# Kernel optimization log

Measured on AMD Instinct MI355X. Metric: run time of the kernel, lower is better.

## Reference

```python
import jax, jax.numpy as jnp
import numpy as np

NUM_HEADS = 4
NUM_GROUPS = 8
EPS = 1e-5


def setup_inputs() -> dict:
    key = jax.random.key(0)
    ks = jax.random.split(key, 4)
    B, C, H, W = 4, 256, 64, 64
    x = jax.random.normal(ks[0], (B, C, H, W), dtype=jnp.float32)
    gamma = jnp.ones((C,), dtype=jnp.float32)
    beta = jnp.zeros((C,), dtype=jnp.float32)
    w_qkv = jax.random.normal(ks[1], (3 * C, C), dtype=jnp.float32) * 0.02
    b_qkv = jnp.zeros((3 * C,), dtype=jnp.float32)
    w_proj = jax.random.normal(ks[2], (C, C), dtype=jnp.float32) * 0.02
    b_proj = jnp.zeros((C,), dtype=jnp.float32)
    return {"x": x, "gamma": gamma, "beta": beta, "w_qkv": w_qkv,
            "b_qkv": b_qkv, "w_proj": w_proj, "b_proj": b_proj}


def _group_norm(x, gamma, beta):
    B, C, H, W = x.shape
    xg = x.reshape(B, NUM_GROUPS, C // NUM_GROUPS, H, W)
    mean = xg.mean(axis=(2, 3, 4), keepdims=True)
    var = xg.var(axis=(2, 3, 4), keepdims=True)
    xn = ((xg - mean) * jax.lax.rsqrt(var + EPS)).reshape(B, C, H, W)
    return xn * gamma[None, :, None, None] + beta[None, :, None, None]


def reference(x, gamma, beta, w_qkv, b_qkv, w_proj, b_proj):
    B, C, H, W = x.shape
    d = C // NUM_HEADS
    scale = d ** (-0.5)
    xn = _group_norm(x, gamma, beta)
    # 1x1 conv == per-pixel linear: (B,C,H,W) x (3C,C) -> (B,3C,H,W)
    qkv = jnp.einsum('bchw,oc->bohw', xn, w_qkv) + b_qkv[None, :, None, None]
    q, k, v = jnp.split(qkv, 3, axis=1)
    S = H * W
    q = q.reshape(B, NUM_HEADS, d, S)  # (B,h,d,S)
    k = k.reshape(B, NUM_HEADS, d, S)
    v = v.reshape(B, NUM_HEADS, d, S)
    # attn scores: q^T k, scaled AFTER the matmul (as in source)
    attn = jax.nn.softmax(jnp.einsum('bhds,bhdt->bhst', q, k) * scale, axis=-1)
    # out = attn @ v^T -> (B,h,S,d) then transpose to (B,h,d,S) -> (B,C,H,W)
    out = jnp.einsum('bhst,bhdt->bhds', attn, v).reshape(B, C, H, W)
    y = jnp.einsum('bchw,oc->bohw', out, w_proj) + b_proj[None, :, None, None]
    return x + y
```

## Files before the change

### kernel.cpp

```cpp
#include <hip/hip_runtime.h>
#include <hip/hip_bf16.h>


typedef __attribute__((ext_vector_type(8))) short          b16x8;
typedef __attribute__((ext_vector_type(4))) float          f32x4;
typedef __attribute__((ext_vector_type(4))) unsigned short u16x4;
typedef __attribute__((ext_vector_type(8))) unsigned short u16x8;

#define SWZ(row, chunk) (((chunk) ^ ((row) & 7)))

__device__ __forceinline__ unsigned short f2bf(float f) {
    union { float f; unsigned u; } v; v.f = f;
    unsigned r = v.u + 0x7FFF + ((v.u >> 16) & 1);
    return (unsigned short)(r >> 16);
}

__device__ __forceinline__ float bf2f(unsigned short u) {
    union { unsigned u; float f; } v; v.u = ((unsigned)u) << 16;
    return v.f;
}

__device__ __forceinline__ unsigned bfpack_trunc(float lo, float hi) {
    union { float f; unsigned u; } a, b;
    a.f = hi; b.f = lo;
    return __builtin_amdgcn_perm(a.u, b.u, 0x07060302u);
}

__device__ __forceinline__ float fexp2(float x) {
#if __has_builtin(__builtin_amdgcn_exp2f)
    return __builtin_amdgcn_exp2f(x);
#else
    return exp2f(x);
#endif
}

__device__ __forceinline__ float frcp(float x) {
#if __has_builtin(__builtin_amdgcn_rcpf)
    return __builtin_amdgcn_rcpf(x);
#else
    return 1.f / x;
#endif
}

__device__ __forceinline__ void gll16(const void* g, void* l) {
    __builtin_amdgcn_global_load_lds(
        (const __attribute__((address_space(1))) unsigned int*)g,
        (__attribute__((address_space(3))) unsigned int*)l, 16, 0, 0);
}

__global__ __launch_bounds__(256) void gn_prepack(const float* __restrict__ x,
                                                  float* __restrict__ partials,
                                                  const float* __restrict__ wqkv,
                                                  const float* __restrict__ bqkv,
                                                  unsigned short* __restrict__ wsw,
                                                  float* __restrict__ bq_pre,
                                                  const float* __restrict__ wproj,
                                                  unsigned short* __restrict__ wswp) {
    int bx = blockIdx.x;
    int t = threadIdx.x;
    if (bx < 512) {
        int bg = bx >> 4, part = bx & 15;
        const float* xp = x + (size_t)bg * 131072 + (size_t)part * 8192;
        float s = 0.f, ss = 0.f;
        for (int k = 0; k < 8; k++) {
            float4 v = *(const float4*)(xp + t * 4 + k * 1024);
            s += v.x + v.y + v.z + v.w;
            ss += v.x * v.x + v.y * v.y + v.z * v.z + v.w * v.w;
        }
        for (int off = 32; off; off >>= 1) {
            s += __shfl_down(s, off);
            ss += __shfl_down(ss, off);
        }
        __shared__ float rs[4], rss[4];
        if ((t & 63) == 0) { rs[t >> 6] = s; rss[t >> 6] = ss; }
        __syncthreads();
        if (t == 0) {
            partials[2 * bx]     = rs[0] + rs[1] + rs[2] + rs[3];
            partials[2 * bx + 1] = rss[0] + rss[1] + rss[2] + rss[3];
        }
    } else if (bx < 608) {
        int gid = (bx - 512) * 256 + t;
        const float qs = 0.125f * 1.44269504f;
        int o = gid >> 5, ch = gid & 31, cblk = ch >> 3, chl = ch & 7;
        float sc = (o < 256) ? qs : 1.f;
        const float* src = &wqkv[o * 256 + ch * 8];
        u16x8 v;
        for (int i = 0; i < 8; i++) v[i] = f2bf(src[i] * sc);
        *(u16x8*)&wsw[((cblk * 768 + o) << 6) + SWZ(o, chl) * 8] = v;
        if (gid < 768) bq_pre[gid] = bqkv[gid] * ((gid < 256) ? qs : 1.f);
    } else {
        int gid = (bx - 608) * 256 + t;
        int o = gid >> 5, ch = gid & 31, cblk = ch >> 3, chl = ch & 7;
        const float* src = &wproj[o * 256 + ch * 8];
        u16x8 v;
        for (int i = 0; i < 8; i++) v[i] = f2bf(src[i]);
        *(u16x8*)&wswp[((cblk * 256 + o) << 6) + SWZ(o, chl) * 8] = v;
    }
}

__global__ __launch_bounds__(256) void qkv_gemm(const float* __restrict__ x,
                                                const float* __restrict__ gamma,
                                                const float* __restrict__ beta,
                                                const unsigned short* __restrict__ wsw,
                                                const float* __restrict__ bq_pre,
                                                const float* __restrict__ partials,
                                                unsigned short* __restrict__ qT,
                                                unsigned short* __restrict__ kT,
                                                unsigned short* __restrict__ vT) {
    __shared__ __align__(16) unsigned short Asm[256 * 64];
    __shared__ __align__(16) unsigned short Bsm[64 * 72];
    __shared__ float stats_s[16];
    int s0 = blockIdx.x * 64, sec = blockIdx.y, b = blockIdx.z;
    int t = threadIdx.x, lane = t & 63, wv = t >> 6;
    int l15 = lane & 15, quad = lane >> 4;
    f32x4 acc[4][4] = {};

    if (t < 8) {
        float s = 0.f, ss = 0.f;
        for (int p = 0; p < 16; p++) {
            s  += partials[2 * ((b * 8 + t) * 16 + p)];
            ss += partials[2 * ((b * 8 + t) * 16 + p) + 1];
        }
        const float invN = 1.f / 131072.f;
        float mean = s * invN;
        float var = ss * invN - mean * mean;
        stats_s[2 * t] = mean;
        stats_s[2 * t + 1] = rsqrtf(var + 1e-5f);
    }

    int tc = t >> 5;
    int ts = (t & 31) * 2;

    for (int k0 = 0; k0 < 256; k0 += 64) {
        int cblk = k0 >> 6;
        __syncthreads();
        const unsigned short* asrc = wsw + (((size_t)cblk * 768 + sec * 256) << 6);
        for (int j = 0; j < 8; j++) {
            int blk = wv * 8 + j;
            gll16(asrc + blk * 512 + lane * 8, &Asm[blk * 512]);
        }
        {
            int cbase = k0 + tc * 8;
            int g = cbase >> 5;
            float mean = stats_s[2 * g], rstd = stats_s[2 * g + 1];
            u16x8 r0, r1;
            for (int ci = 0; ci < 8; ci++) {
                int c = cbase + ci;
                float2 xv = *(const float2*)&x[((size_t)(b * 256 + c)) * 4096 + s0 + ts];
                float ga = gamma[c] * rstd, be = beta[c] - mean * gamma[c] * rstd;
                r0[ci] = (short)f2bf(xv.x * ga + be);
                r1[ci] = (short)f2bf(xv.y * ga + be);
            }
            *(u16x8*)&Bsm[(ts + 0) * 72 + tc * 8] = r0;
            *(u16x8*)&Bsm[(ts + 1) * 72 + tc * 8] = r1;
        }
        __syncthreads();
        for (int kc = 0; kc < 2; kc++) {
            b16x8 bb[4];
            for (int nn = 0; nn < 4; nn++)
                bb[nn] = *(const b16x8*)(Bsm + (nn * 16 + l15) * 72 + kc * 32 + quad * 8);
            for (int ot = 0; ot < 4; ot++) {
                int row = wv * 16 + l15;
                b16x8 a = *(const b16x8*)&Asm[(ot * 64 + row) * 64 + SWZ(row, kc * 4 + quad) * 8];
                for (int nn = 0; nn < 4; nn++)
                    acc[ot][nn] = __builtin_amdgcn_mfma_f32_16x16x32_bf16(a, bb[nn], acc[ot][nn], 0, 0, 0);
            }
        }
    }

    if (sec < 2) {
        unsigned short* dstT = (sec == 0) ? qT : kT;
        int ddbase = wv * 16 + quad * 4;
        for (int ot = 0; ot < 4; ot++) {
            unsigned short* dst = dstT + (size_t)(b * 4 + ot) * 4096 * 64;
            for (int nn = 0; nn < 4; nn++) {
                int s = s0 + nn * 16 + l15;
                u16x4 pv;
                for (int r = 0; r < 4; r++)
                    pv[r] = f2bf(acc[ot][nn][r] + bq_pre[sec * 256 + ot * 64 + ddbase + r]);
                *(u16x4*)&dst[(size_t)s * 64 + SWZ(s, ddbase >> 3) * 8 + (ddbase & 7)] = pv;
            }
        }
    } else {
        int kt = blockIdx.x;
        for (int ot = 0; ot < 4; ot++) {
            int bh = b * 4 + ot;
            for (int r = 0; r < 4; r++) {
                int dd = wv * 16 + quad * 4 + r;
                float bs = bq_pre[512 + ot * 64 + dd];
                u16x4 pv = { f2bf(acc[ot][0][r] + bs), f2bf(acc[ot][1][r] + bs),
                             f2bf(acc[ot][2][r] + bs), f2bf(acc[ot][3][r] + bs) };
                size_t off = ((size_t)(bh * 64 + kt) * 64 + dd) * 64
                           + SWZ(dd, l15 >> 1) * 8 + (l15 & 1) * 4;
                *(u16x4*)&vT[off] = pv;
            }
        }
    }
}

__global__ __launch_bounds__(128, 2) void attn_kernel(const unsigned short* __restrict__ qT,
                                                      const unsigned short* __restrict__ kT,
                                                      const unsigned short* __restrict__ vT,
                                                      unsigned short* __restrict__ Opart,
                                                      float* __restrict__ lsum) {
    __shared__ __align__(16) unsigned short QP[128 * 64];
    __shared__ __align__(16) unsigned short Ksm[2][64 * 64];
    int bx = blockIdx.x;
    int q0 = (bx >> 1) * 128;
    int half = bx & 1;
    int kt0 = half * 32, ktN = kt0 + 32;
    int h = blockIdx.y, b = blockIdx.z;
    int bh = b * 4 + h, slab = bh * 2 + half;
    int t = threadIdx.x, lane = t & 63, wv = t >> 6;
    int l15 = lane & 15, quad = lane >> 4;

    const unsigned short* qTb = qT + (size_t)bh * 4096 * 64;
    const unsigned short* kTb = kT + (size_t)bh * 4096 * 64;
    const unsigned short* vTb = vT + (size_t)bh * 64 * 4096;

    for (int j = 0; j < 12; j++) {
        int i = wv + 2 * j;
        if (i < 16) {
            gll16(qTb + (size_t)q0 * 64 + i * 512 + lane * 8, &QP[i * 512]);
        } else {
            int ii = i - 16;
            gll16(kTb + (size_t)kt0 * 4096 + ii * 512 + lane * 8, &Ksm[0][ii * 512]);
        }
    }
    __syncthreads();

    b16x8 aq[4][2];
    for (int mt = 0; mt < 4; mt++)
        for (int kc = 0; kc < 2; kc++) {
            int row = wv * 64 + mt * 16 + l15;
            aq[mt][kc] = *(const b16x8*)&QP[row * 64 + SWZ(row, kc * 4 + quad) * 8];
        }

    f32x4 O[4][4] = {};
    float ls[4][4] = {};

    for (int kt = kt0; kt < ktN; kt++) {
        int cur = kt & 1;
        int nb = cur ^ 1;
        bool more = (kt < ktN - 1);
        if (more) {
            for (int j = 0; j < 4; j++) {
                int blk = wv * 4 + j;
                gll16(kTb + (size_t)(kt + 1) * 4096 + blk * 512 + lane * 8,
                      &Ksm[nb][blk * 512]);
            }
        }

        f32x4 sc[4][4] = {};
        for (int kc = 0; kc < 2; kc++) {
            b16x8 bk[4];
            for (int nk = 0; nk < 4; nk++) {
                int row = nk * 16 + l15;
                bk[nk] = *(const b16x8*)&Ksm[cur][row * 64 + SWZ(l15, kc * 4 + quad) * 8];
            }
            for (int mt = 0; mt < 4; mt++)
                for (int nk = 0; nk < 4; nk++)
                    sc[mt][nk] = __builtin_amdgcn_mfma_f32_16x16x32_bf16(
                        aq[mt][kc], bk[nk], sc[mt][nk], 0, 0, 0);
        }

        for (int mt = 0; mt < 4; mt++) {
            for (int r = 0; r < 4; r++) {
                float p0 = fexp2(sc[mt][0][r]);
                float p1 = fexp2(sc[mt][1][r]);
                float p2 = fexp2(sc[mt][2][r]);
                float p3 = fexp2(sc[mt][3][r]);
                ls[mt][r] += (p0 + p1) + (p2 + p3);
                int row = wv * 64 + mt * 16 + quad * 4 + r;
                u16x4 pk;
                pk[0] = (unsigned short)(bfpack_trunc(p0, p1) & 0xFFFF);
                union { unsigned u[2]; u16x4 v; } pku;
                pku.u[0] = bfpack_trunc(p0, p1);
                pku.u[1] = bfpack_trunc(p2, p3);
                *(u16x4*)&QP[row * 64 + SWZ(row, l15 >> 1) * 8 + (l15 & 1) * 4] = pku.v;
            }
        }

        for (int kc = 0; kc < 2; kc++) {
            b16x8 ap[4], bv[4];
            for (int mt = 0; mt < 4; mt++) {
                int row = wv * 64 + mt * 16 + l15;
                ap[mt] = *(const b16x8*)&QP[row * 64 + SWZ(row, kc * 4 + quad) * 8];
            }
            for (int nf = 0; nf < 4; nf++) {
                int row = nf * 16 + l15;
                bv[nf] = *(const b16x8*)&vTb[(size_t)kt * 4096 + row * 64
                                             + SWZ(l15, kc * 4 + quad) * 8];
            }
            for (int mt = 0; mt < 4; mt++)
                for (int nf = 0; nf < 4; nf++)
                    O[mt][nf] = __builtin_amdgcn_mfma_f32_16x16x32_bf16(
                        ap[mt], bv[nf], O[mt][nf], 0, 0, 0);
        }

        __syncthreads();
    }

    for (int mt = 0; mt < 4; mt++)
        for (int r = 0; r < 4; r++) {
            float s = ls[mt][r];
            for (int off = 1; off < 16; off <<= 1) s += __shfl_xor(s, off);
            int srow = q0 + wv * 64 + mt * 16 + quad * 4 + r;
            if (l15 == 0) lsum[(size_t)slab * 4096 + srow] = s;
        }

    for (int mt = 0; mt < 4; mt++)
        for (int nf = 0; nf < 4; nf++)
            for (int r = 0; r < 4; r++) {
                int s = q0 + wv * 64 + mt * 16 + quad * 4 + r;
                int d = nf * 16 + l15;
                Opart[((size_t)slab * 4096 + s) * 64 + d] = f2bf(O[mt][nf][r]);
            }
}

__global__ __launch_bounds__(256) void proj_gemm(const unsigned short* __restrict__ Opart,
                                                 const float* __restrict__ lsum,
                                                 const unsigned short* __restrict__ wswp,
                                                 const float* __restrict__ bias,
                                                 const float* __restrict__ x,
                                                 float* __restrict__ out) {
    __shared__ __align__(16) unsigned short Asm[64 * 64];
    __shared__ __align__(16) unsigned short Bsm[64 * 72];
    int s0 = blockIdx.x * 64, o0 = blockIdx.y * 64, b = blockIdx.z;
    int t = threadIdx.x, lane = t & 63, wv = t >> 6;
    int l15 = lane & 15, quad = lane >> 4;
    int rl = t >> 2;
    f32x4 acc[4] = {};
    for (int k0 = 0; k0 < 256; k0 += 64) {
        int cblk = k0 >> 6;
        __syncthreads();
        const unsigned short* asrc = wswp + (((size_t)cblk * 256 + o0) << 6);
        for (int j = 0; j < 2; j++) {
            int blk = wv * 2 + j;
            gll16(asrc + blk * 512 + lane * 8, &Asm[blk * 512]);
        }
        {
            int bh = b * 4 + cblk;
            int s = s0 + rl;
            float l0 = lsum[(size_t)(bh * 2 + 0) * 4096 + s];
            float l1 = lsum[(size_t)(bh * 2 + 1) * 4096 + s];
            float rcp = frcp(l0 + l1);
            for (int j = 0; j < 2; j++) {
                int off = (t & 3) * 16 + j * 8;
                u16x8 o0v = *(const u16x8*)&Opart[((size_t)(bh * 2 + 0) * 4096 + s) * 64 + off];
                u16x8 o1v = *(const u16x8*)&Opart[((size_t)(bh * 2 + 1) * 4096 + s) * 64 + off];
                u16x8 res;
                for (int i = 0; i < 8; i++)
                    res[i] = f2bf((bf2f(o0v[i]) + bf2f(o1v[i])) * rcp);
                *(u16x8*)&Bsm[rl * 72 + off] = res;
            }
        }
        __syncthreads();
        for (int kc = 0; kc < 2; kc++) {
            int row = wv * 16 + l15;
            b16x8 a = *(const b16x8*)&Asm[row * 64 + SWZ(row, kc * 4 + quad) * 8];
            for (int nn = 0; nn < 4; nn++) {
                b16x8 bb = *(const b16x8*)(Bsm + (nn * 16 + l15) * 72 + kc * 32 + quad * 8);
                acc[nn] = __builtin_amdgcn_mfma_f32_16x16x32_bf16(a, bb, acc[nn], 0, 0, 0);
            }
        }
    }
    for (int nn = 0; nn < 4; nn++) {
        for (int r = 0; r < 4; r++) {
            int o = o0 + wv * 16 + quad * 4 + r;
            int s = s0 + nn * 16 + l15;
            size_t idx = ((size_t)(b * 256 + o)) * 4096 + s;
            out[idx] = acc[nn][r] + bias[o] + x[idx];
        }
    }
}

extern "C" void kernel_launch(void* const* d_in, const int* in_sizes, int n_in,
                              void* d_out, int out_size, void* d_ws, size_t ws_size,
                              hipStream_t stream) {
    const float* x      = (const float*)d_in[0];
    const float* gamma  = (const float*)d_in[1];
    const float* beta   = (const float*)d_in[2];
    const float* w_qkv  = (const float*)d_in[3];
    const float* b_qkv  = (const float*)d_in[4];
    const float* w_proj = (const float*)d_in[5];
    const float* b_proj = (const float*)d_in[6];
    float* out = (float*)d_out;

    unsigned short* ws = (unsigned short*)d_ws;
    unsigned short* qT    = ws;
    unsigned short* kT    = qT + (size_t)16 * 4096 * 64;
    unsigned short* vT    = kT + (size_t)16 * 4096 * 64;
    unsigned short* scratch = vT + (size_t)16 * 4096 * 64;
    unsigned short* Opart = scratch + (size_t)4 * 4096 * 256;
    float*          lsump = (float*)(Opart + (size_t)32 * 4096 * 64);
    unsigned short* wqkv_sw = (unsigned short*)lsump;
    float*          bq_pre  = (float*)((char*)lsump + 393216);
    float*          partials = (float*)scratch;
    unsigned short* wproj_sw = scratch + 32768;

    hipLaunchKernelGGL(gn_prepack,  dim3(640),      dim3(256), 0, stream,
                       x, partials, w_qkv, b_qkv, wqkv_sw, bq_pre, w_proj, wproj_sw);
    hipLaunchKernelGGL(qkv_gemm,    dim3(64, 3, 4), dim3(256), 0, stream,
                       x, gamma, beta, wqkv_sw, bq_pre, partials, qT, kT, vT);
    hipLaunchKernelGGL(attn_kernel, dim3(64, 4, 4), dim3(128), 0, stream,
                       qT, kT, vT, Opart, lsump);
    hipLaunchKernelGGL(proj_gemm,   dim3(64, 4, 4), dim3(256), 0, stream,
                       Opart, lsump, wproj_sw, b_proj, x, out);
}
```

Baseline: 181.6 us.

## Precompute normalized bf16 activations in separate kernel, stream into QKV GEMM via async loads

Adds an xn_prep kernel that applies group norm once and writes bf16 activations in a swizzled, transposed layout, reusing the Opart buffer. The QKV GEMM then loads its B tile with direct global-to-LDS loads instead of reading fp32 x and normalizing it in every section block. Before, each of the three sections repeated the normalization and conversion. This costs an extra kernel launch and an extra round trip of the activation tensor through memory. A dead local variable in the attention kernel is also removed.

New measurement: 187.5 us. 1.03x slower.

```diff
diff --git a/kernel.cpp b/kernel.cpp
--- a/kernel.cpp
+++ b/kernel.cpp
@@ -98,23 +98,15 @@
     }
 }
 
-__global__ __launch_bounds__(256) void qkv_gemm(const float* __restrict__ x,
-                                                const float* __restrict__ gamma,
-                                                const float* __restrict__ beta,
-                                                const unsigned short* __restrict__ wsw,
-                                                const float* __restrict__ bq_pre,
-                                                const float* __restrict__ partials,
-                                                unsigned short* __restrict__ qT,
-                                                unsigned short* __restrict__ kT,
-                                                unsigned short* __restrict__ vT) {
-    __shared__ __align__(16) unsigned short Asm[256 * 64];
-    __shared__ __align__(16) unsigned short Bsm[64 * 72];
+__global__ __launch_bounds__(256) void xn_prep(const float* __restrict__ x,
+                                               const float* __restrict__ gamma,
+                                               const float* __restrict__ beta,
+                                               const float* __restrict__ partials,
+                                               unsigned short* __restrict__ xnT) {
     __shared__ float stats_s[16];
-    int s0 = blockIdx.x * 64, sec = blockIdx.y, b = blockIdx.z;
-    int t = threadIdx.x, lane = t & 63, wv = t >> 6;
-    int l15 = lane & 15, quad = lane >> 4;
-    f32x4 acc[4][4] = {};
-
+    int st = blockIdx.x;
+    int b = blockIdx.y;
+    int t = threadIdx.x;
     if (t < 8) {
         float s = 0.f, ss = 0.f;
         for (int p = 0; p < 16; p++) {
@@ -127,9 +119,36 @@
         stats_s[2 * t] = mean;
         stats_s[2 * t + 1] = rsqrtf(var + 1e-5f);
     }
-
+    __syncthreads();
+    int s = st * 32 + (t & 31);
     int tc = t >> 5;
-    int ts = (t & 31) * 2;
+    for (int cblk = 0; cblk < 4; cblk++) {
+        int cbase = cblk * 64 + tc * 8;
+        int g = cbase >> 5;
+        float mean = stats_s[2 * g], rstd = stats_s[2 * g + 1];
+        u16x8 r0;
+        for (int ci = 0; ci < 8; ci++) {
+            int c = cbase + ci;
+            float xv = x[((size_t)(b * 256 + c)) * 4096 + s];
+            float ga = gamma[c] * rstd, be = beta[c] - mean * gamma[c] * rstd;
+            r0[ci] = (short)f2bf(xv * ga + be);
+        }
+        *(u16x8*)&xnT[((size_t)(b * 4 + cblk) * 4096 + s) * 64 + SWZ(s, tc) * 8] = r0;
+    }
+}
+
+__global__ __launch_bounds__(256) void qkv_gemm(const unsigned short* __restrict__ xnT,
+                                                const unsigned short* __restrict__ wsw,
+                                                const float* __restrict__ bq_pre,
+                                                unsigned short* __restrict__ qT,
+                                                unsigned short* __restrict__ kT,
+                                                unsigned short* __restrict__ vT) {
+    __shared__ __align__(16) unsigned short Asm[256 * 64];
+    __shared__ __align__(16) unsigned short Bsm[64 * 64];
+    int s0 = blockIdx.x * 64, sec = blockIdx.y, b = blockIdx.z;
+    int t = threadIdx.x, lane = t & 63, wv = t >> 6;
+    int l15 = lane & 15, quad = lane >> 4;
+    f32x4 acc[4][4] = {};
 
     for (int k0 = 0; k0 < 256; k0 += 64) {
         int cblk = k0 >> 6;
@@ -139,26 +158,18 @@
             int blk = wv * 8 + j;
             gll16(asrc + blk * 512 + lane * 8, &Asm[blk * 512]);
         }
-        {
-            int cbase = k0 + tc * 8;
-            int g = cbase >> 5;
-            float mean = stats_s[2 * g], rstd = stats_s[2 * g + 1];
-            u16x8 r0, r1;
-            for (int ci = 0; ci < 8; ci++) {
-                int c = cbase + ci;
-                float2 xv = *(const float2*)&x[((size_t)(b * 256 + c)) * 4096 + s0 + ts];
-                float ga = gamma[c] * rstd, be = beta[c] - mean * gamma[c] * rstd;
-                r0[ci] = (short)f2bf(xv.x * ga + be);
-                r1[ci] = (short)f2bf(xv.y * ga + be);
-            }
-            *(u16x8*)&Bsm[(ts + 0) * 72 + tc * 8] = r0;
-            *(u16x8*)&Bsm[(ts + 1) * 72 + tc * 8] = r1;
+        const unsigned short* bsrc = xnT + ((size_t)(b * 4 + cblk) * 4096 + s0) * 64;
+        for (int j = 0; j < 2; j++) {
+            int blk = wv * 2 + j;
+            gll16(bsrc + blk * 512 + lane * 8, &Bsm[blk * 512]);
         }
         __syncthreads();
         for (int kc = 0; kc < 2; kc++) {
             b16x8 bb[4];
-            for (int nn = 0; nn < 4; nn++)
-                bb[nn] = *(const b16x8*)(Bsm + (nn * 16 + l15) * 72 + kc * 32 + quad * 8);
+            for (int nn = 0; nn < 4; nn++) {
+                int row = nn * 16 + l15;
+                bb[nn] = *(const b16x8*)&Bsm[row * 64 + SWZ(row, kc * 4 + quad) * 8];
+            }
             for (int ot = 0; ot < 4; ot++) {
                 int row = wv * 16 + l15;
                 b16x8 a = *(const b16x8*)&Asm[(ot * 64 + row) * 64 + SWZ(row, kc * 4 + quad) * 8];
@@ -272,8 +283,6 @@
                 float p3 = fexp2(sc[mt][3][r]);
                 ls[mt][r] += (p0 + p1) + (p2 + p3);
                 int row = wv * 64 + mt * 16 + quad * 4 + r;
-                u16x4 pk;
-                pk[0] = (unsigned short)(bfpack_trunc(p0, p1) & 0xFFFF);
                 union { unsigned u[2]; u16x4 v; } pku;
                 pku.u[0] = bfpack_trunc(p0, p1);
                 pku.u[1] = bfpack_trunc(p2, p3);
@@ -398,11 +407,14 @@
     float*          bq_pre  = (float*)((char*)lsump + 393216);
     float*          partials = (float*)scratch;
     unsigned short* wproj_sw = scratch + 32768;
+    unsigned short* xnT      = Opart;
 
     hipLaunchKernelGGL(gn_prepack,  dim3(640),      dim3(256), 0, stream,
                        x, partials, w_qkv, b_qkv, wqkv_sw, bq_pre, w_proj, wproj_sw);
+    hipLaunchKernelGGL(xn_prep,     dim3(128, 4),   dim3(256), 0, stream,
+                       x, gamma, beta, partials, xnT);
     hipLaunchKernelGGL(qkv_gemm,    dim3(64, 3, 4), dim3(256), 0, stream,
-                       x, gamma, beta, wqkv_sw, bq_pre, partials, qT, kT, vT);
+                       xnT, wqkv_sw, bq_pre, qT, kT, vT);
     hipLaunchKernelGGL(attn_kernel, dim3(64, 4, 4), dim3(128), 0, stream,
                        qT, kT, vT, Opart, lsump);
     hipLaunchKernelGGL(proj_gemm,   dim3(64, 4, 4), dim3(256), 0, stream,
```
